# Optimization experiments

Measured on AMD Instinct MI355X. Metric: run time of the kernel, lower is better.

The kernel has to match this reference:

```python
import jax, jax.numpy as jnp
import numpy as np

B = 4; S_L = 512; WIN = 256; SCH = 3; CCH = 128; F = 8; P = 4; RNN = 128; FC = 256
L1 = (WIN - F + 1) // P          # after conv1 + pool1
L2 = (L1 - F + 1) // P           # after conv2 + pool2
D1 = L2 * CCH                    # flattened conv feature dim fed to GRU


def _conv1d(x, w, b):
    # x: (N, W, Cin), w: (F, Cin, Cout), VALID, stride 1 (matches keras Conv1D)
    return jax.lax.conv_general_dilated(x, w, (1,), 'VALID', dimension_numbers=('NWC', 'WIO', 'NWC')) + b


def _maxpool(x, p):
    return jax.lax.reduce_window(x, -jnp.inf, jax.lax.max, (1, p, 1), (1, p, 1), 'VALID')


def _gru(x, h0, mask, W, U, b):
    # keras GRU v2 (reset_after=True). b[0]=input bias, b[1]=recurrent bias.
    # Masked steps carry state through (keras semantics: output==state for GRU).
    u = U.shape[0]
    xg = x @ W + b[0]  # (B, T, 3u) precomputed input projections
    br = b[1]

    def step(h, inp):
        xt, mt = inp  # (B, 3u), (B,)
        rg = h @ U + br
        z = jax.nn.sigmoid(xt[:, :u] + rg[:, :u])
        r = jax.nn.sigmoid(xt[:, u:2 * u] + rg[:, u:2 * u])
        hh = jnp.tanh(xt[:, 2 * u:] + r * rg[:, 2 * u:])
        hn = z * h + (1.0 - z) * hh
        hn = jnp.where(mt[:, None], hn, h)
        return hn, hn

    _, ys = jax.lax.scan(step, h0, (jnp.swapaxes(xg, 0, 1), jnp.swapaxes(mask, 0, 1)))
    return jnp.swapaxes(ys, 0, 1)  # (B, T, u)


def _bidir(x, m, hf, hb, Wf, Uf, bf, Wb, Ub, bb):
    # Bidirectional(merge='concat'); backward layer sees reversed inputs+mask,
    # its output is reversed back to align with time (keras behaviour).
    yf = _gru(x, hf, m, Wf, Uf, bf)
    yb = _gru(x[:, ::-1], hb, m[:, ::-1], Wb, Ub, bb)[:, ::-1]
    return jnp.concatenate([yf, yb], axis=-1)


def _forward(x, state1_f, state1_b, state2_f, state2_b,
             conv1_w, conv1_b, conv2_w, conv2_b,
             g1f_W, g1f_U, g1f_b, g1b_W, g1b_U, g1b_b,
             g2f_W, g2f_U, g2f_b, g2b_W, g2b_U, g2b_b,
             d1_w, d1_b, d2_w, d2_b, d3_w, d3_b, m):
    bsz = x.shape[0]
    h = x.reshape(bsz * S_L, WIN, SCH)
    h = _maxpool(jax.nn.leaky_relu(_conv1d(h, conv1_w, conv1_b), 0.2), P)
    h = _maxpool(jax.nn.leaky_relu(_conv1d(h, conv2_w, conv2_b), 0.2), P)
    h = h.reshape(bsz, S_L, D1)
    h = _bidir(h, m, state1_f, state1_b, g1f_W, g1f_U, g1f_b, g1b_W, g1b_U, g1b_b)
    h = _bidir(h, m, state2_f, state2_b, g2f_W, g2f_U, g2f_b, g2b_W, g2b_U, g2b_b)
    # keras layers.Attention(use_scale=False): dot-product self attention,
    # key mask -> -1e9 on scores, query mask -> zero outputs.
    scores = jnp.einsum('btd,bsd->bts', h, h)
    scores = jnp.where(m[:, None, :], scores, -1e9)
    h = jnp.einsum('bts,bsd->btd', jax.nn.softmax(scores, axis=-1), h)
    h = h * m[:, :, None].astype(h.dtype)
    h = jax.nn.leaky_relu(h @ d1_w + d1_b, 0.2)   # dropout is identity at inference
    h = jax.nn.leaky_relu(h @ d2_w + d2_b, 0.2)
    return (h @ d3_w + d3_b)[..., 0]              # squeeze -> (B, s_l)


def setup_inputs() -> dict:
    key = jax.random.key(0)
    ks = jax.random.split(key, 32)
    g = lambda k, s: jax.random.normal(k, s, jnp.float32) * 0.05
    inp = {}
    inp['x'] = jax.random.normal(ks[0], (B, S_L, WIN, SCH), jnp.float32)
    inp['m'] = jax.random.randint(ks[1], (B, S_L), 0, 2) > 0
    inp['state1_f'] = jax.random.uniform(ks[2], (B, RNN), jnp.float32, -1.0, 1.0)
    inp['state1_b'] = jax.random.uniform(ks[3], (B, RNN), jnp.float32, -1.0, 1.0)
    inp['state2_f'] = jax.random.uniform(ks[4], (B, RNN), jnp.float32, -1.0, 1.0)
    inp['state2_b'] = jax.random.uniform(ks[5], (B, RNN), jnp.float32, -1.0, 1.0)
    inp['conv1_w'] = g(ks[6], (F, SCH, CCH)); inp['conv1_b'] = jnp.zeros((CCH,), jnp.float32)
    inp['conv2_w'] = g(ks[7], (F, CCH, CCH)); inp['conv2_b'] = jnp.zeros((CCH,), jnp.float32)
    i = 8
    for nm, din in (('g1f', D1), ('g1b', D1), ('g2f', 2 * RNN), ('g2b', 2 * RNN)):
        inp[nm + '_W'] = g(ks[i], (din, 3 * RNN))
        inp[nm + '_U'] = g(ks[i + 1], (RNN, 3 * RNN))
        inp[nm + '_b'] = jnp.zeros((2, 3 * RNN), jnp.float32)
        i += 2
    inp['d1_w'] = g(ks[i], (2 * RNN, FC)); inp['d1_b'] = jnp.zeros((FC,), jnp.float32)
    inp['d2_w'] = g(ks[i + 1], (FC, FC)); inp['d2_b'] = jnp.zeros((FC,), jnp.float32)
    inp['d3_w'] = g(ks[i + 2], (FC, 1)); inp['d3_b'] = jnp.zeros((1,), jnp.float32)
    return inp


def reference(x, m, state1_f, state1_b, state2_f, state2_b,
              conv1_w, conv1_b, conv2_w, conv2_b,
              g1f_W, g1f_U, g1f_b, g1b_W, g1b_U, g1b_b,
              g2f_W, g2f_U, g2f_b, g2b_W, g2b_U, g2b_b,
              d1_w, d1_b, d2_w, d2_b, d3_w, d3_b):
    return _forward(x, state1_f, state1_b, state2_f, state2_b,
                    conv1_w, conv1_b, conv2_w, conv2_b,
                    g1f_W, g1f_U, g1f_b, g1b_W, g1b_U, g1b_b,
                    g2f_W, g2f_U, g2f_b, g2b_W, g2b_U, g2b_b,
                    d1_w, d1_b, d2_w, d2_b, d3_w, d3_b, m)
```

## Files before the change

### kernel.cpp

```cpp
#include <hip/hip_runtime.h>

#define LRELU(v) ((v) > 0.f ? (v) : 0.2f * (v))

typedef float f32x4 __attribute__((ext_vector_type(4)));
typedef __bf16 bf16x8 __attribute__((ext_vector_type(8)));
typedef unsigned short ushort8v __attribute__((ext_vector_type(8)));

__device__ __forceinline__ unsigned short f2bf(float f) {
    unsigned int u = __float_as_uint(f);
    u += 0x7fffu + ((u >> 16) & 1u);
    return (unsigned short)(u >> 16);
}
__device__ __forceinline__ float bf2f(unsigned short h) {
    return __uint_as_float(((unsigned int)h) << 16);
}
__device__ __forceinline__ float sigmoid_fast(float x) {
    float e = __builtin_amdgcn_exp2f(-x * 1.442695041f);
    return __builtin_amdgcn_rcpf(1.f + e);
}
__device__ __forceinline__ float tanh_fast(float x) {
    float e = __builtin_amdgcn_exp2f(x * 2.885390082f);
    return 1.f - 2.f * __builtin_amdgcn_rcpf(e + 1.f);
}
__device__ __forceinline__ float dpp_add_xor1(float v) {
    int r = __builtin_amdgcn_mov_dpp(__float_as_int(v), 0xB1, 0xF, 0xF, true);
    return v + __int_as_float(r);
}
__device__ __forceinline__ float dpp_add_xor2(float v) {
    int r = __builtin_amdgcn_mov_dpp(__float_as_int(v), 0x4E, 0xF, 0xF, true);
    return v + __int_as_float(r);
}

__global__ void mask_decode_kernel(const unsigned int* __restrict__ mraw,
                                   int* __restrict__ mi) {
    __shared__ int is_u8;
    if (threadIdx.x == 0) {
        int u8 = 0;
        for (int i = 0; i < 512; i++) {
            if (mraw[i] > 1u) { u8 = 1; break; }
        }
        is_u8 = u8;
    }
    __syncthreads();
    if (is_u8) {
        const unsigned char* b8 = (const unsigned char*)mraw;
        for (int i = threadIdx.x; i < 2048; i += blockDim.x) mi[i] = b8[i] ? 1 : 0;
    } else {
        for (int i = threadIdx.x; i < 2048; i += blockDim.x) mi[i] = mraw[i] ? 1 : 0;
    }
}

__global__ __launch_bounds__(256) void prepack_w2(const float* __restrict__ w2,
                                                  unsigned short* __restrict__ bth,
                                                  unsigned short* __restrict__ btl) {
    int idx = blockIdx.x * 256 + threadIdx.x;
    int c = idx >> 10, k = idx & 1023;
    float v = w2[k * 128 + c];
    unsigned short hi = f2bf(v);
    unsigned short lo = f2bf(v - bf2f(hi));
    bth[(long)c * 1024 + k] = hi;
    btl[(long)c * 1024 + k] = lo;
}

__global__ __launch_bounds__(256) void prepack_wt(const float* __restrict__ W,
                                                  unsigned short* __restrict__ h,
                                                  unsigned short* __restrict__ l,
                                                  int K, int N) {
    long idx = (long)blockIdx.x * 256 + threadIdx.x;
    if (idx >= (long)K * N) return;
    int n = (int)(idx / K), k = (int)(idx % K);
    float v = W[(long)k * N + n];
    unsigned short hi = f2bf(v);
    unsigned short lo = f2bf(v - bf2f(hi));
    h[idx] = hi;
    l[idx] = lo;
}

__global__ __launch_bounds__(256) void conv_kernel(
    const float* __restrict__ x, const float* __restrict__ w1,
    const float* __restrict__ b1, const unsigned short* __restrict__ bth,
    const unsigned short* __restrict__ btl, const float* __restrict__ b2,
    float* __restrict__ feat) {
    __shared__ float xs[3][256];
    __shared__ __align__(16) unsigned short p1h[72 * 128];
    __shared__ __align__(16) unsigned short p1l[72 * 128];
    long s = blockIdx.x;
    int tid = threadIdx.x;
    const float* xp = x + s * 768;
    for (int i = tid; i < 768; i += 256) xs[i % 3][i / 3] = xp[i];
    for (int i = tid; i < 10 * 128; i += 256) {
        p1h[62 * 128 + i] = 0;
        p1l[62 * 128 + i] = 0;
    }
    __syncthreads();

    {
        int ch = tid & 127;
        int half = tid >> 7;
        float w1r[24];
#pragma unroll
        for (int fc = 0; fc < 24; fc++) w1r[fc] = w1[fc * 128 + ch];
        float bias1 = b1[ch];
        for (int po = half; po < 62; po += 2) {
            int p0 = po * 4;
            float a0 = bias1, a1 = bias1, a2 = bias1, a3 = bias1;
#pragma unroll
            for (int c = 0; c < 3; c++) {
                float xv[11];
#pragma unroll
                for (int q = 0; q < 11; q++) xv[q] = xs[c][p0 + q];
#pragma unroll
                for (int f = 0; f < 8; f++) {
                    float w = w1r[f * 3 + c];
                    a0 = fmaf(xv[f + 0], w, a0);
                    a1 = fmaf(xv[f + 1], w, a1);
                    a2 = fmaf(xv[f + 2], w, a2);
                    a3 = fmaf(xv[f + 3], w, a3);
                }
            }
            float m01 = fmaxf(LRELU(a0), LRELU(a1));
            float m23 = fmaxf(LRELU(a2), LRELU(a3));
            float v = fmaxf(m01, m23);
            unsigned short hi = f2bf(v);
            unsigned short lo = f2bf(v - bf2f(hi));
            int cs = ch ^ ((po & 7) << 3);
            p1h[po * 128 + cs] = hi;
            p1l[po * 128 + cs] = lo;
        }
    }
    __syncthreads();

    const int l = tid & 63, w = tid >> 6;
    const int r = l & 15, g = l >> 4;
    f32x4 acc[4][2];
    const f32x4 zz = {0.f, 0.f, 0.f, 0.f};
#pragma unroll
    for (int m = 0; m < 4; m++) {
        acc[m][0] = zz;
        acc[m][1] = zz;
    }
#pragma unroll 2
    for (int ks = 0; ks < 32; ks++) {
        const int f = ks >> 2;
        const int cin0 = ((ks & 3) << 5) + (g << 3);
        bf16x8 bh[2], bl[2];
#pragma unroll
        for (int n = 0; n < 2; n++) {
            const int c = ((w << 1) + n) * 16 + r;
            const long bo = (long)c * 1024 + (ks << 5) + (g << 3);
            bh[n] = __builtin_bit_cast(bf16x8, *(const ushort8v*)(bth + bo));
            bl[n] = __builtin_bit_cast(bf16x8, *(const ushort8v*)(btl + bo));
        }
        bf16x8 ah[4], al[4];
#pragma unroll
        for (int m = 0; m < 4; m++) {
            const int row = m * 16 + r + f;
            const int col = cin0 ^ ((row & 7) << 3);
            const int off = row * 128 + col;
            ah[m] = __builtin_bit_cast(bf16x8, *(const ushort8v*)(p1h + off));
            al[m] = __builtin_bit_cast(bf16x8, *(const ushort8v*)(p1l + off));
        }
#pragma unroll
        for (int m = 0; m < 4; m++) {
#pragma unroll
            for (int n = 0; n < 2; n++) {
                acc[m][n] = __builtin_amdgcn_mfma_f32_16x16x32_bf16(ah[m], bh[n], acc[m][n], 0, 0, 0);
                acc[m][n] = __builtin_amdgcn_mfma_f32_16x16x32_bf16(ah[m], bl[n], acc[m][n], 0, 0, 0);
                acc[m][n] = __builtin_amdgcn_mfma_f32_16x16x32_bf16(al[m], bh[n], acc[m][n], 0, 0, 0);
            }
        }
    }
#pragma unroll
    for (int m = 0; m < 4; m++) {
        const int j = m * 4 + g;
        if (j < 13) {
#pragma unroll
            for (int n = 0; n < 2; n++) {
                const int ch = ((w << 1) + n) * 16 + r;
                const float bias = b2[ch];
                float v0 = LRELU(acc[m][n].x + bias);
                float v1 = LRELU(acc[m][n].y + bias);
                float v2 = LRELU(acc[m][n].z + bias);
                float v3 = LRELU(acc[m][n].w + bias);
                feat[s * 1664 + j * 128 + ch] = fmaxf(fmaxf(v0, v1), fmaxf(v2, v3));
            }
        }
    }
}

template <int ACT>
__global__ __launch_bounds__(256) void gemm_bf16(
    const float* __restrict__ A, const unsigned short* __restrict__ Wth,
    const unsigned short* __restrict__ Wtl, const float* __restrict__ bias,
    float* __restrict__ C, int M, int N, int K) {
    __shared__ __align__(16) unsigned short Ah[64 * 40];
    __shared__ __align__(16) unsigned short Al[64 * 40];
    const int tid = threadIdx.x;
    const int w = tid >> 6, l = tid & 63, r = l & 15, g = l >> 4;
    const int m0 = blockIdx.y * 64, n0 = blockIdx.x * 64;
    const int col = n0 + w * 16 + r;
    const int srow = tid >> 2, sgq = tid & 3;
    f32x4 acc[4];
    const f32x4 zz = {0.f, 0.f, 0.f, 0.f};
#pragma unroll
    for (int m = 0; m < 4; m++) acc[m] = zz;

    const float* ap0 = A + (long)(m0 + srow) * K + sgq * 8;
    const long bbase = (long)col * K + g * 8;
    float4 v0 = *(const float4*)ap0;
    float4 v1 = *(const float4*)(ap0 + 4);
    ushort8v bhc = *(const ushort8v*)(Wth + bbase);
    ushort8v blc = *(const ushort8v*)(Wtl + bbase);

    for (int k0 = 0; k0 < K; k0 += 32) {
        float4 nv0, nv1;
        ushort8v nbh, nbl;
        if (k0 + 32 < K) {
            nv0 = *(const float4*)(ap0 + k0 + 32);
            nv1 = *(const float4*)(ap0 + k0 + 36);
            nbh = *(const ushort8v*)(Wth + bbase + k0 + 32);
            nbl = *(const ushort8v*)(Wtl + bbase + k0 + 32);
        }
        float vv[8] = {v0.x, v0.y, v0.z, v0.w, v1.x, v1.y, v1.z, v1.w};
        ushort8v hh, ll;
#pragma unroll
        for (int q = 0; q < 8; q++) {
            unsigned short h16 = f2bf(vv[q]);
            hh[q] = h16;
            ll[q] = f2bf(vv[q] - bf2f(h16));
        }
        const int slot = sgq ^ (srow & 3);
        __syncthreads();
        *(ushort8v*)&Ah[srow * 40 + slot * 8] = hh;
        *(ushort8v*)&Al[srow * 40 + slot * 8] = ll;
        __syncthreads();
        bf16x8 bh = __builtin_bit_cast(bf16x8, bhc);
        bf16x8 bl = __builtin_bit_cast(bf16x8, blc);
#pragma unroll
        for (int m = 0; m < 4; m++) {
            const int arow = m * 16 + r;
            const int aoff = arow * 40 + ((g ^ (arow & 3)) << 3);
            bf16x8 ah = __builtin_bit_cast(bf16x8, *(const ushort8v*)(Ah + aoff));
            bf16x8 al = __builtin_bit_cast(bf16x8, *(const ushort8v*)(Al + aoff));
            acc[m] = __builtin_amdgcn_mfma_f32_16x16x32_bf16(ah, bh, acc[m], 0, 0, 0);
            acc[m] = __builtin_amdgcn_mfma_f32_16x16x32_bf16(ah, bl, acc[m], 0, 0, 0);
            acc[m] = __builtin_amdgcn_mfma_f32_16x16x32_bf16(al, bh, acc[m], 0, 0, 0);
        }
        v0 = nv0; v1 = nv1; bhc = nbh; blc = nbl;
    }
    const float bv = bias ? bias[col] : 0.f;
#pragma unroll
    for (int m = 0; m < 4; m++) {
#pragma unroll
        for (int q = 0; q < 4; q++) {
            const int row = m0 + m * 16 + g * 4 + q;
            float v = acc[m][q] + bv;
            if (ACT == 1) v = LRELU(v);
            C[(long)row * N + col] = v;
        }
    }
}

template <int ACT>
__global__ __launch_bounds__(256) void gemm_nn(
    const float* __restrict__ A, long sA, const float* __restrict__ B, long sB,
    const float* __restrict__ bias, const int* __restrict__ qmask,
    float* __restrict__ C, long sC, int M, int N, int K) {
    int bz = blockIdx.z;
    A += (long)bz * sA;
    B += (long)bz * sB;
    C += (long)bz * sC;
    __shared__ __align__(16) float As[16][68];
    __shared__ __align__(16) float Bs[16][68];
    int tid = threadIdx.x;
    int tm = tid >> 4, tn = tid & 15;
    int m0 = blockIdx.y * 64, n0 = blockIdx.x * 64;
    int la_m = tid & 63, la_k = (tid >> 6) * 4;
    int lb_k = tid >> 4, lb_n = (tid & 15) * 4;
    float acc[4][4] = {};
    for (int k0 = 0; k0 < K; k0 += 16) {
        float4 av = *(const float4*)&A[(long)(m0 + la_m) * K + k0 + la_k];
        float4 bv = *(const float4*)&B[(long)(k0 + lb_k) * N + n0 + lb_n];
        As[la_k + 0][la_m] = av.x;
        As[la_k + 1][la_m] = av.y;
        As[la_k + 2][la_m] = av.z;
        As[la_k + 3][la_m] = av.w;
        *(float4*)&Bs[lb_k][lb_n] = bv;
        __syncthreads();
#pragma unroll
        for (int k = 0; k < 16; k++) {
            float4 a4 = *(const float4*)&As[k][tm * 4];
            float4 b4 = *(const float4*)&Bs[k][tn * 4];
            float aa[4] = {a4.x, a4.y, a4.z, a4.w};
            float bb[4] = {b4.x, b4.y, b4.z, b4.w};
#pragma unroll
            for (int i = 0; i < 4; i++)
#pragma unroll
                for (int j = 0; j < 4; j++) acc[i][j] = fmaf(aa[i], bb[j], acc[i][j]);
        }
        __syncthreads();
    }
#pragma unroll
    for (int i = 0; i < 4; i++) {
        int row = m0 + tm * 4 + i;
        float msc = qmask ? (float)qmask[(long)bz * M + row] : 1.f;
#pragma unroll
        for (int j = 0; j < 4; j++) {
            int col = n0 + tn * 4 + j;
            float v = acc[i][j] + (bias ? bias[col] : 0.f);
            if (ACT == 1) v = LRELU(v);
            C[(long)row * N + col] = v * msc;
        }
    }
}

__global__ __launch_bounds__(256) void scores_kernel(
    const float* __restrict__ h, const int* __restrict__ mask,
    float* __restrict__ S) {
    int bz = blockIdx.z;
    const float* A = h + (long)bz * 512 * 256;
    float* C = S + (long)bz * 512 * 512;
    __shared__ __align__(16) float As[16][68];
    __shared__ __align__(16) float Bs[16][68];
    int tid = threadIdx.x;
    int tm = tid >> 4, tn = tid & 15;
    int m0 = blockIdx.y * 64, n0 = blockIdx.x * 64;
    int lr = tid & 63, lk = (tid >> 6) * 4;
    float acc[4][4] = {};
    for (int k0 = 0; k0 < 256; k0 += 16) {
        float4 av = *(const float4*)&A[(long)(m0 + lr) * 256 + k0 + lk];
        float4 bv = *(const float4*)&A[(long)(n0 + lr) * 256 + k0 + lk];
        As[lk + 0][lr] = av.x;
        As[lk + 1][lr] = av.y;
        As[lk + 2][lr] = av.z;
        As[lk + 3][lr] = av.w;
        Bs[lk + 0][lr] = bv.x;
        Bs[lk + 1][lr] = bv.y;
        Bs[lk + 2][lr] = bv.z;
        Bs[lk + 3][lr] = bv.w;
        __syncthreads();
#pragma unroll
        for (int k = 0; k < 16; k++) {
            float4 a4 = *(const float4*)&As[k][tm * 4];
            float4 b4 = *(const float4*)&Bs[k][tn * 4];
            float aa[4] = {a4.x, a4.y, a4.z, a4.w};
            float bb[4] = {b4.x, b4.y, b4.z, b4.w};
#pragma unroll
            for (int i = 0; i < 4; i++)
#pragma unroll
                for (int j = 0; j < 4; j++) acc[i][j] = fmaf(aa[i], bb[j], acc[i][j]);
        }
        __syncthreads();
    }
#pragma unroll
    for (int i = 0; i < 4; i++) {
        int t = m0 + tm * 4 + i;
#pragma unroll
        for (int j = 0; j < 4; j++) {
            int ss = n0 + tn * 4 + j;
            C[(long)t * 512 + ss] = mask[bz * 512 + ss] ? acc[i][j] : -1e9f;
        }
    }
}

__global__ __launch_bounds__(256) void softmax_kernel(float* __restrict__ S) {
    long row = blockIdx.x;
    float* p = S + row * 512;
    int tid = threadIdx.x;
    __shared__ float red[8];
    float v0 = p[tid], v1 = p[tid + 256];
    float mx = fmaxf(v0, v1);
#pragma unroll
    for (int off = 32; off; off >>= 1) mx = fmaxf(mx, __shfl_down(mx, off));
    if ((tid & 63) == 0) red[tid >> 6] = mx;
    __syncthreads();
    mx = fmaxf(fmaxf(red[0], red[1]), fmaxf(red[2], red[3]));
    float e0 = expf(v0 - mx), e1 = expf(v1 - mx);
    float sm = e0 + e1;
#pragma unroll
    for (int off = 32; off; off >>= 1) sm += __shfl_down(sm, off);
    if ((tid & 63) == 0) red[4 + (tid >> 6)] = sm;
    __syncthreads();
    float inv = 1.f / (red[4] + red[5] + red[6] + red[7]);
    p[tid] = e0 * inv;
    p[tid + 256] = e1 * inv;
}

__global__ __launch_bounds__(512, 2) void gru_kernel(
    const float* __restrict__ xgf, const float* __restrict__ xgb,
    const float* __restrict__ Uf, const float* __restrict__ Ub,
    const float* __restrict__ brf, const float* __restrict__ brb,
    const float* __restrict__ h0f, const float* __restrict__ h0b,
    const int* __restrict__ mask, float* __restrict__ out) {
    int b = blockIdx.x & 3;
    int dir = blockIdx.x >> 2;
    const float* __restrict__ xg = dir ? xgb : xgf;
    const float* __restrict__ U = dir ? Ub : Uf;
    const float* __restrict__ br = dir ? brb : brf;
    const float* __restrict__ h0 = dir ? h0b : h0f;
    const int tid = threadIdx.x;
    const int c = tid >> 2;
    const int kq = tid & 3;

    __shared__ __align__(16) float xs[2][16 * 384];
    __shared__ __align__(16) float hsh[2][144];
    __shared__ unsigned long long mwords[8];

    auto stage = [&](int cc, int bufi) {
#pragma unroll
        for (int i = 0; i < 3; i++) {
            int g = i * 512 + tid;
            int j = g / 96;
            int col = (g - j * 96) * 4;
            int ts = cc * 16 + j;
            int t = dir ? (511 - ts) : ts;
            const float* src = xg + ((long)(b * 512 + t)) * 384 + col;
            __builtin_amdgcn_global_load_lds(
                (const __attribute__((address_space(1))) void*)src,
                (__attribute__((address_space(3))) void*)&xs[bufi][g * 4], 16, 0, 0);
        }
    };
    stage(0, 0);

    f32x4 u4[3][8];
#pragma unroll
    for (int g = 0; g < 3; g++)
#pragma unroll
        for (int q = 0; q < 8; q++) {
            const float* up = U + (long)(kq * 32 + q * 4) * 384 + g * 128 + c;
            u4[g][q].x = up[0];
            u4[g][q].y = up[384];
            u4[g][q].z = up[768];
            u4[g][q].w = up[1152];
        }
    float br3[3];
#pragma unroll
    for (int g = 0; g < 3; g++) br3[g] = br[g * 128 + c];

    float hreg = h0[b * 128 + c];
    if (kq == 0) hsh[0][c + (c >> 5) * 4] = hreg;
    if (tid < 64) {
#pragma unroll
        for (int w = 0; w < 8; w++) {
            int idx = w * 64 + tid;
            int t = dir ? (511 - idx) : idx;
            unsigned long long bm = __ballot(mask[b * 512 + t] != 0);
            if (tid == 0) mwords[w] = bm;
        }
    }
    asm volatile("s_waitcnt lgkmcnt(0)" ::: "memory");
    __builtin_amdgcn_s_barrier();

    int cur = 0;
    for (int cc = 0; cc < 32; cc++) {
        asm volatile("s_waitcnt vmcnt(0)" ::: "memory");
        if (cc < 31) stage(cc + 1, (cc + 1) & 1);
#pragma unroll
        for (int g = 0; g < 3; g++)
#pragma unroll
            for (int q = 0; q < 8; q++) asm volatile("" : "+v"(u4[g][q]));
        __builtin_amdgcn_s_barrier();
        const float* xb = xs[cc & 1];
        unsigned mwbits = (unsigned)((mwords[cc >> 2] >> ((cc & 3) * 16)) & 0xffffull);
#pragma unroll 1
        for (int jj = 0; jj < 16; jj++) {
            int step = cc * 16 + jj;
            int t = dir ? (511 - step) : step;
            long obase = ((long)(b * 512 + t)) * 256 + dir * 128;
            if ((mwbits >> jj) & 1) {
                const float* hp = &hsh[cur][kq * 36];
                float az0 = 0.f, az1 = 0.f, ar0 = 0.f, ar1 = 0.f, ah0 = 0.f, ah1 = 0.f;
#pragma unroll
                for (int q = 0; q < 8; q++) {
                    float4 h4 = *(const float4*)(hp + q * 4);
                    az0 = fmaf(h4.x, u4[0][q].x, az0);
                    az1 = fmaf(h4.y, u4[0][q].y, az1);
                    az0 = fmaf(h4.z, u4[0][q].z, az0);
                    az1 = fmaf(h4.w, u4[0][q].w, az1);
                    ar0 = fmaf(h4.x, u4[1][q].x, ar0);
                    ar1 = fmaf(h4.y, u4[1][q].y, ar1);
                    ar0 = fmaf(h4.z, u4[1][q].z, ar0);
                    ar1 = fmaf(h4.w, u4[1][q].w, ar1);
                    ah0 = fmaf(h4.x, u4[2][q].x, ah0);
                    ah1 = fmaf(h4.y, u4[2][q].y, ah1);
                    ah0 = fmaf(h4.z, u4[2][q].z, ah0);
                    ah1 = fmaf(h4.w, u4[2][q].w, ah1);
                }
                float rgz = dpp_add_xor2(dpp_add_xor1(az0 + az1));
                float rgr = dpp_add_xor2(dpp_add_xor1(ar0 + ar1));
                float rgh = dpp_add_xor2(dpp_add_xor1(ah0 + ah1));
                if (kq == 0) {
                    float xz = xb[jj * 384 + c];
                    float xr = xb[jj * 384 + 128 + c];
                    float xh = xb[jj * 384 + 256 + c];
                    float z = sigmoid_fast(xz + rgz + br3[0]);
                    float r_ = sigmoid_fast(xr + rgr + br3[1]);
                    float hc = tanh_fast(fmaf(r_, rgh + br3[2], xh));
                    float hn = fmaf(z, hreg - hc, hc);
                    hreg = hn;
                    hsh[cur ^ 1][c + (c >> 5) * 4] = hn;
                    out[obase + c] = hn;
                }
                asm volatile("s_waitcnt lgkmcnt(0)" ::: "memory");
                __builtin_amdgcn_s_barrier();
                cur ^= 1;
            } else {
                if (kq == 0) out[obase + c] = hreg;
            }
        }
    }
}

__global__ __launch_bounds__(256) void final_kernel(
    const float* __restrict__ fc2, const float* __restrict__ w,
    const float* __restrict__ b, float* __restrict__ out) {
    int row = blockIdx.x * 4 + (threadIdx.x >> 6);
    int lane = threadIdx.x & 63;
    const float* a = fc2 + (long)row * 256;
    float acc = 0.f;
#pragma unroll
    for (int i = 0; i < 4; i++) acc = fmaf(a[lane + i * 64], w[lane + i * 64], acc);
#pragma unroll
    for (int off = 32; off; off >>= 1) acc += __shfl_down(acc, off);
    if (lane == 0) out[row] = acc + b[0];
}

extern "C" void kernel_launch(void* const* d_in, const int* in_sizes, int n_in,
                              void* d_out, int out_size, void* d_ws,
                              size_t ws_size, hipStream_t stream) {
    const float* x = (const float*)d_in[0];
    const unsigned int* mraw = (const unsigned int*)d_in[1];
    const float* s1f = (const float*)d_in[2];
    const float* s1b = (const float*)d_in[3];
    const float* s2f = (const float*)d_in[4];
    const float* s2b = (const float*)d_in[5];
    const float* c1w = (const float*)d_in[6];
    const float* c1b = (const float*)d_in[7];
    const float* c2w = (const float*)d_in[8];
    const float* c2b = (const float*)d_in[9];
    const float* g1fW = (const float*)d_in[10];
    const float* g1fU = (const float*)d_in[11];
    const float* g1fb = (const float*)d_in[12];
    const float* g1bW = (const float*)d_in[13];
    const float* g1bU = (const float*)d_in[14];
    const float* g1bb = (const float*)d_in[15];
    const float* g2fW = (const float*)d_in[16];
    const float* g2fU = (const float*)d_in[17];
    const float* g2fb = (const float*)d_in[18];
    const float* g2bW = (const float*)d_in[19];
    const float* g2bU = (const float*)d_in[20];
    const float* g2bb = (const float*)d_in[21];
    const float* d1w = (const float*)d_in[22];
    const float* d1b = (const float*)d_in[23];
    const float* d2w = (const float*)d_in[24];
    const float* d2b = (const float*)d_in[25];
    const float* d3w = (const float*)d_in[26];
    const float* d3b = (const float*)d_in[27];
    float* out = (float*)d_out;

    float* ws = (float*)d_ws;
    size_t off = 0;
    auto take = [&](size_t n) {
        float* p = ws + off;
        off += (n + 63) & ~(size_t)63;
        return p;
    };
    int* mask_i = (int*)take(2048);
    float* feat = take(2048UL * 1664);
    float* xg1f = take(2048UL * 384);
    float* xg1b = take(2048UL * 384);
    float* gru1 = take(2048UL * 256);
    float* xg2f = take(2048UL * 384);
    float* xg2b = take(2048UL * 384);
    float* gru2 = take(2048UL * 256);
    float* sc = take(4UL * 512 * 512);
    float* attn = take(2048UL * 256);
    float* fc1 = take(2048UL * 256);
    float* fc2 = take(2048UL * 256);
    unsigned short* bth = (unsigned short*)take(65536);
    unsigned short* btl = (unsigned short*)take(65536);
    unsigned short* wt1fh = (unsigned short*)take(319488);
    unsigned short* wt1fl = (unsigned short*)take(319488);
    unsigned short* wt1bh = (unsigned short*)take(319488);
    unsigned short* wt1bl = (unsigned short*)take(319488);
    unsigned short* wt2fh = (unsigned short*)take(49152);
    unsigned short* wt2fl = (unsigned short*)take(49152);
    unsigned short* wt2bh = (unsigned short*)take(49152);
    unsigned short* wt2bl = (unsigned short*)take(49152);

    mask_decode_kernel<<<1, 256, 0, stream>>>(mraw, mask_i);
    prepack_w2<<<512, 256, 0, stream>>>(c2w, bth, btl);
    prepack_wt<<<2496, 256, 0, stream>>>(g1fW, wt1fh, wt1fl, 1664, 384);
    prepack_wt<<<2496, 256, 0, stream>>>(g1bW, wt1bh, wt1bl, 1664, 384);
    prepack_wt<<<384, 256, 0, stream>>>(g2fW, wt2fh, wt2fl, 256, 384);
    prepack_wt<<<384, 256, 0, stream>>>(g2bW, wt2bh, wt2bl, 256, 384);
    conv_kernel<<<2048, 256, 0, stream>>>(x, c1w, c1b, bth, btl, c2b, feat);

    gemm_bf16<0><<<dim3(6, 32), 256, 0, stream>>>(feat, wt1fh, wt1fl, g1fb,
                                                  xg1f, 2048, 384, 1664);
    gemm_bf16<0><<<dim3(6, 32), 256, 0, stream>>>(feat, wt1bh, wt1bl, g1bb,
                                                  xg1b, 2048, 384, 1664);
    gru_kernel<<<8, 512, 0, stream>>>(xg1f, xg1b, g1fU, g1bU, g1fb + 384,
                                      g1bb + 384, s1f, s1b, mask_i, gru1);

    gemm_bf16<0><<<dim3(6, 32), 256, 0, stream>>>(gru1, wt2fh, wt2fl, g2fb,
                                                  xg2f, 2048, 384, 256);
    gemm_bf16<0><<<dim3(6, 32), 256, 0, stream>>>(gru1, wt2bh, wt2bl, g2bb,
                                                  xg2b, 2048, 384, 256);
    gru_kernel<<<8, 512, 0, stream>>>(xg2f, xg2b, g2fU, g2bU, g2fb + 384,
                                      g2bb + 384, s2f, s2b, mask_i, gru2);

    scores_kernel<<<dim3(8, 8, 4), 256, 0, stream>>>(gru2, mask_i, sc);
    softmax_kernel<<<2048, 256, 0, stream>>>(sc);
    gemm_nn<0><<<dim3(4, 8, 4), 256, 0, stream>>>(sc, 512L * 512, gru2, 512L * 256,
                                                  nullptr, mask_i, attn, 512L * 256,
                                                  512, 256, 512);

    gemm_nn<1><<<dim3(4, 32, 1), 256, 0, stream>>>(attn, 0, d1w, 0, d1b, nullptr,
                                                   fc1, 0, 2048, 256, 256);
    gemm_nn<1><<<dim3(4, 32, 1), 256, 0, stream>>>(fc1, 0, d2w, 0, d2b, nullptr,
                                                   fc2, 0, 2048, 256, 256);
    final_kernel<<<512, 256, 0, stream>>>(fc2, d3w, d3b, out);
}
```

Before: 774.3 us.

## Halve GRU block size, two hidden units per thread with prepacked U

The recurrent GRU kernel now runs 256 threads per block instead of 512, and each thread computes two hidden columns (c and c+64), holding 48 float4 of U in registers. A new prepack kernel reorders U into a per-thread contiguous layout so each thread can load its slice with vector loads. The aim is cheaper per-step barriers and fewer waves to synchronise on the serial recurrence. The cost is higher register pressure (192 VGPRs for U alone), more serial FMA work per thread, and four extra prepack launches.

```diff
diff --git a/kernel.cpp b/kernel.cpp
--- a/kernel.cpp
+++ b/kernel.cpp
@@ -74,6 +74,17 @@
     unsigned short lo = f2bf(v - bf2f(hi));
     h[idx] = hi;
     l[idx] = lo;
+}
+
+__global__ __launch_bounds__(256) void prepack_ugru(const float* __restrict__ U,
+                                                    float* __restrict__ up) {
+    int idx = blockIdx.x * 256 + threadIdx.x;
+    if (idx >= 49152) return;
+    int tid = idx / 192, rem = idx % 192;
+    int g = rem >> 6, rem2 = rem & 63;
+    int p = rem2 >> 5, j = rem2 & 31;
+    int c = tid >> 2, kq = tid & 3;
+    up[idx] = U[(long)(kq * 32 + j) * 384 + g * 128 + p * 64 + c];
 }
 
 __global__ __launch_bounds__(256) void conv_kernel(
@@ -386,16 +397,16 @@
     p[tid + 256] = e1 * inv;
 }
 
-__global__ __launch_bounds__(512, 2) void gru_kernel(
+__global__ __launch_bounds__(256, 1) void gru_kernel(
     const float* __restrict__ xgf, const float* __restrict__ xgb,
-    const float* __restrict__ Uf, const float* __restrict__ Ub,
+    const float* __restrict__ Upf, const float* __restrict__ Upb,
     const float* __restrict__ brf, const float* __restrict__ brb,
     const float* __restrict__ h0f, const float* __restrict__ h0b,
     const int* __restrict__ mask, float* __restrict__ out) {
     int b = blockIdx.x & 3;
     int dir = blockIdx.x >> 2;
     const float* __restrict__ xg = dir ? xgb : xgf;
-    const float* __restrict__ U = dir ? Ub : Uf;
+    const float* __restrict__ Up = dir ? Upb : Upf;
     const float* __restrict__ br = dir ? brb : brf;
     const float* __restrict__ h0 = dir ? h0b : h0f;
     const int tid = threadIdx.x;
@@ -408,8 +419,8 @@
 
     auto stage = [&](int cc, int bufi) {
 #pragma unroll
-        for (int i = 0; i < 3; i++) {
-            int g = i * 512 + tid;
+        for (int i = 0; i < 6; i++) {
+            int g = i * 256 + tid;
             int j = g / 96;
             int col = (g - j * 96) * 4;
             int ts = cc * 16 + j;
@@ -422,23 +433,28 @@
     };
     stage(0, 0);
 
-    f32x4 u4[3][8];
-#pragma unroll
-    for (int g = 0; g < 3; g++)
-#pragma unroll
-        for (int q = 0; q < 8; q++) {
-            const float* up = U + (long)(kq * 32 + q * 4) * 384 + g * 128 + c;
-            u4[g][q].x = up[0];
-            u4[g][q].y = up[384];
-            u4[g][q].z = up[768];
-            u4[g][q].w = up[1152];
-        }
-    float br3[3];
-#pragma unroll
-    for (int g = 0; g < 3; g++) br3[g] = br[g * 128 + c];
-
-    float hreg = h0[b * 128 + c];
-    if (kq == 0) hsh[0][c + (c >> 5) * 4] = hreg;
+    f32x4 u4[48];
+    {
+        const f32x4* up = (const f32x4*)(Up + (long)tid * 192);
+#pragma unroll
+        for (int q = 0; q < 48; q++) u4[q] = up[q];
+    }
+#pragma unroll
+    for (int q = 0; q < 48; q++) asm volatile("" : "+v"(u4[q]));
+
+    float brv[6], hregp[2];
+#pragma unroll
+    for (int g = 0; g < 3; g++) {
+        brv[g * 2 + 0] = br[g * 128 + c];
+        brv[g * 2 + 1] = br[g * 128 + 64 + c];
+    }
+    hregp[0] = h0[b * 128 + c];
+    hregp[1] = h0[b * 128 + 64 + c];
+    if (kq == 0) {
+        hsh[0][c + (c >> 5) * 4] = hregp[0];
+        int c1 = c + 64;
+        hsh[0][c1 + (c1 >> 5) * 4] = hregp[1];
+    }
     if (tid < 64) {
 #pragma unroll
         for (int w = 0; w < 8; w++) {
@@ -455,10 +471,6 @@
     for (int cc = 0; cc < 32; cc++) {
         asm volatile("s_waitcnt vmcnt(0)" ::: "memory");
         if (cc < 31) stage(cc + 1, (cc + 1) & 1);
-#pragma unroll
-        for (int g = 0; g < 3; g++)
-#pragma unroll
-            for (int q = 0; q < 8; q++) asm volatile("" : "+v"(u4[g][q]));
         __builtin_amdgcn_s_barrier();
         const float* xb = xs[cc & 1];
         unsigned mwbits = (unsigned)((mwords[cc >> 2] >> ((cc & 3) * 16)) & 0xffffull);
@@ -469,43 +481,62 @@
             long obase = ((long)(b * 512 + t)) * 256 + dir * 128;
             if ((mwbits >> jj) & 1) {
                 const float* hp = &hsh[cur][kq * 36];
-                float az0 = 0.f, az1 = 0.f, ar0 = 0.f, ar1 = 0.f, ah0 = 0.f, ah1 = 0.f;
+                float s0 = 0.f, s1 = 0.f, s2 = 0.f, s3 = 0.f, s4 = 0.f, s5 = 0.f;
 #pragma unroll
                 for (int q = 0; q < 8; q++) {
                     float4 h4 = *(const float4*)(hp + q * 4);
-                    az0 = fmaf(h4.x, u4[0][q].x, az0);
-                    az1 = fmaf(h4.y, u4[0][q].y, az1);
-                    az0 = fmaf(h4.z, u4[0][q].z, az0);
-                    az1 = fmaf(h4.w, u4[0][q].w, az1);
-                    ar0 = fmaf(h4.x, u4[1][q].x, ar0);
-                    ar1 = fmaf(h4.y, u4[1][q].y, ar1);
-                    ar0 = fmaf(h4.z, u4[1][q].z, ar0);
-                    ar1 = fmaf(h4.w, u4[1][q].w, ar1);
-                    ah0 = fmaf(h4.x, u4[2][q].x, ah0);
-                    ah1 = fmaf(h4.y, u4[2][q].y, ah1);
-                    ah0 = fmaf(h4.z, u4[2][q].z, ah0);
-                    ah1 = fmaf(h4.w, u4[2][q].w, ah1);
+                    f32x4 uz0 = u4[q], uz1 = u4[8 + q];
+                    f32x4 ur0 = u4[16 + q], ur1 = u4[24 + q];
+                    f32x4 uh0 = u4[32 + q], uh1 = u4[40 + q];
+                    s0 = fmaf(h4.x, uz0.x, s0); s0 = fmaf(h4.y, uz0.y, s0);
+                    s0 = fmaf(h4.z, uz0.z, s0); s0 = fmaf(h4.w, uz0.w, s0);
+                    s1 = fmaf(h4.x, uz1.x, s1); s1 = fmaf(h4.y, uz1.y, s1);
+                    s1 = fmaf(h4.z, uz1.z, s1); s1 = fmaf(h4.w, uz1.w, s1);
+                    s2 = fmaf(h4.x, ur0.x, s2); s2 = fmaf(h4.y, ur0.y, s2);
+                    s2 = fmaf(h4.z, ur0.z, s2); s2 = fmaf(h4.w, ur0.w, s2);
+                    s3 = fmaf(h4.x, ur1.x, s3); s3 = fmaf(h4.y, ur1.y, s3);
+                    s3 = fmaf(h4.z, ur1.z, s3); s3 = fmaf(h4.w, ur1.w, s3);
+                    s4 = fmaf(h4.x, uh0.x, s4); s4 = fmaf(h4.y, uh0.y, s4);
+                    s4 = fmaf(h4.z, uh0.z, s4); s4 = fmaf(h4.w, uh0.w, s4);
+                    s5 = fmaf(h4.x, uh1.x, s5); s5 = fmaf(h4.y, uh1.y, s5);
+                    s5 = fmaf(h4.z, uh1.z, s5); s5 = fmaf(h4.w, uh1.w, s5);
                 }
-                float rgz = dpp_add_xor2(dpp_add_xor1(az0 + az1));
-                float rgr = dpp_add_xor2(dpp_add_xor1(ar0 + ar1));
-                float rgh = dpp_add_xor2(dpp_add_xor1(ah0 + ah1));
+                s0 = dpp_add_xor2(dpp_add_xor1(s0));
+                s1 = dpp_add_xor2(dpp_add_xor1(s1));
+                s2 = dpp_add_xor2(dpp_add_xor1(s2));
+                s3 = dpp_add_xor2(dpp_add_xor1(s3));
+                s4 = dpp_add_xor2(dpp_add_xor1(s4));
+                s5 = dpp_add_xor2(dpp_add_xor1(s5));
                 if (kq == 0) {
-                    float xz = xb[jj * 384 + c];
-                    float xr = xb[jj * 384 + 128 + c];
-                    float xh = xb[jj * 384 + 256 + c];
-                    float z = sigmoid_fast(xz + rgz + br3[0]);
-                    float r_ = sigmoid_fast(xr + rgr + br3[1]);
-                    float hc = tanh_fast(fmaf(r_, rgh + br3[2], xh));
-                    float hn = fmaf(z, hreg - hc, hc);
-                    hreg = hn;
-                    hsh[cur ^ 1][c + (c >> 5) * 4] = hn;
-                    out[obase + c] = hn;
+                    const float* xr0 = xb + jj * 384;
+                    {
+                        float z = sigmoid_fast(xr0[c] + s0 + brv[0]);
+                        float r_ = sigmoid_fast(xr0[128 + c] + s2 + brv[2]);
+                        float hcv = tanh_fast(fmaf(r_, s4 + brv[4], xr0[256 + c]));
+                        float hn = fmaf(z, hregp[0] - hcv, hcv);
+                        hregp[0] = hn;
+                        hsh[cur ^ 1][c + (c >> 5) * 4] = hn;
+                        out[obase + c] = hn;
+                    }
+                    {
+                        int c1 = c + 64;
+                        float z = sigmoid_fast(xr0[c1] + s1 + brv[1]);
+                        float r_ = sigmoid_fast(xr0[128 + c1] + s3 + brv[3]);
+                        float hcv = tanh_fast(fmaf(r_, s5 + brv[5], xr0[256 + c1]));
+                        float hn = fmaf(z, hregp[1] - hcv, hcv);
+                        hregp[1] = hn;
+                        hsh[cur ^ 1][c1 + (c1 >> 5) * 4] = hn;
+                        out[obase + c1] = hn;
+                    }
                 }
                 asm volatile("s_waitcnt lgkmcnt(0)" ::: "memory");
                 __builtin_amdgcn_s_barrier();
                 cur ^= 1;
             } else {
-                if (kq == 0) out[obase + c] = hreg;
+                if (kq == 0) {
+                    out[obase + c] = hregp[0];
+                    out[obase + 64 + c] = hregp[1];
+                }
             }
         }
     }
@@ -587,6 +618,10 @@
     unsigned short* wt2fl = (unsigned short*)take(49152);
     unsigned short* wt2bh = (unsigned short*)take(49152);
     unsigned short* wt2bl = (unsigned short*)take(49152);
+    float* up1f = take(49152);
+    float* up1b = take(49152);
+    float* up2f = take(49152);
+    float* up2b = take(49152);
 
     mask_decode_kernel<<<1, 256, 0, stream>>>(mraw, mask_i);
     prepack_w2<<<512, 256, 0, stream>>>(c2w, bth, btl);
@@ -594,20 +629,24 @@
     prepack_wt<<<2496, 256, 0, stream>>>(g1bW, wt1bh, wt1bl, 1664, 384);
     prepack_wt<<<384, 256, 0, stream>>>(g2fW, wt2fh, wt2fl, 256, 384);
     prepack_wt<<<384, 256, 0, stream>>>(g2bW, wt2bh, wt2bl, 256, 384);
+    prepack_ugru<<<192, 256, 0, stream>>>(g1fU, up1f);
+    prepack_ugru<<<192, 256, 0, stream>>>(g1bU, up1b);
+    prepack_ugru<<<192, 256, 0, stream>>>(g2fU, up2f);
+    prepack_ugru<<<192, 256, 0, stream>>>(g2bU, up2b);
     conv_kernel<<<2048, 256, 0, stream>>>(x, c1w, c1b, bth, btl, c2b, feat);
 
     gemm_bf16<0><<<dim3(6, 32), 256, 0, stream>>>(feat, wt1fh, wt1fl, g1fb,
                                                   xg1f, 2048, 384, 1664);
     gemm_bf16<0><<<dim3(6, 32), 256, 0, stream>>>(feat, wt1bh, wt1bl, g1bb,
                                                   xg1b, 2048, 384, 1664);
-    gru_kernel<<<8, 512, 0, stream>>>(xg1f, xg1b, g1fU, g1bU, g1fb + 384,
+    gru_kernel<<<8, 256, 0, stream>>>(xg1f, xg1b, up1f, up1b, g1fb + 384,
                                       g1bb + 384, s1f, s1b, mask_i, gru1);
 
     gemm_bf16<0><<<dim3(6, 32), 256, 0, stream>>>(gru1, wt2fh, wt2fl, g2fb,
                                                   xg2f, 2048, 384, 256);
     gemm_bf16<0><<<dim3(6, 32), 256, 0, stream>>>(gru1, wt2bh, wt2bl, g2bb,
                                                   xg2b, 2048, 384, 256);
-    gru_kernel<<<8, 512, 0, stream>>>(xg2f, xg2b, g2fU, g2bU, g2fb + 384,
+    gru_kernel<<<8, 256, 0, stream>>>(xg2f, xg2b, up2f, up2b, g2fb + 384,
                                       g2bb + 384, s2f, s2b, mask_i, gru2);
 
     scores_kernel<<<dim3(8, 8, 4), 256, 0, stream>>>(gru2, mask_i, sc);
```

Result: slower. 874.1 us (+12.9%).

## Emit split-bf16 activations from producers and use direct-to-LDS GEMM loads

Applied to the files above, without the earlier changes.

The conv and GRU kernels now write their outputs as pre-split bf16 hi/lo pairs. The GEMM no longer has to convert fp32 A tiles in every k-step, and it loads A straight into LDS with global_load_lds. The fp32 scores kernel is replaced by the same split-bf16 MFMA GEMM with a mask epilogue. In exchange the producers do extra conversion work and writes, and A tile loads are no longer prefetched one step ahead, which may expose load latency.

```diff
diff --git a/kernel.cpp b/kernel.cpp
--- a/kernel.cpp
+++ b/kernel.cpp
@@ -80,7 +80,7 @@
     const float* __restrict__ x, const float* __restrict__ w1,
     const float* __restrict__ b1, const unsigned short* __restrict__ bth,
     const unsigned short* __restrict__ btl, const float* __restrict__ b2,
-    float* __restrict__ feat) {
+    unsigned short* __restrict__ feat_h, unsigned short* __restrict__ feat_l) {
     __shared__ float xs[3][256];
     __shared__ __align__(16) unsigned short p1h[72 * 128];
     __shared__ __align__(16) unsigned short p1l[72 * 128];
@@ -182,19 +182,30 @@
                 float v1 = LRELU(acc[m][n].y + bias);
                 float v2 = LRELU(acc[m][n].z + bias);
                 float v3 = LRELU(acc[m][n].w + bias);
-                feat[s * 1664 + j * 128 + ch] = fmaxf(fmaxf(v0, v1), fmaxf(v2, v3));
+                float v = fmaxf(fmaxf(v0, v1), fmaxf(v2, v3));
+                unsigned short hi = f2bf(v);
+                feat_h[s * 1664 + j * 128 + ch] = hi;
+                feat_l[s * 1664 + j * 128 + ch] = f2bf(v - bf2f(hi));
             }
         }
     }
 }
 
-template <int ACT>
-__global__ __launch_bounds__(256) void gemm_bf16(
-    const float* __restrict__ A, const unsigned short* __restrict__ Wth,
-    const unsigned short* __restrict__ Wtl, const float* __restrict__ bias,
-    float* __restrict__ C, int M, int N, int K) {
-    __shared__ __align__(16) unsigned short Ah[64 * 40];
-    __shared__ __align__(16) unsigned short Al[64 * 40];
+template <int MASK>
+__global__ __launch_bounds__(256) void gemm_bf16v2(
+    const unsigned short* __restrict__ Agh, const unsigned short* __restrict__ Agl,
+    const unsigned short* __restrict__ Bth, const unsigned short* __restrict__ Btl,
+    const float* __restrict__ bias, const int* __restrict__ mask,
+    float* __restrict__ C, long sAz, long sBz, long sCz,
+    int M, int N, int K) {
+    const int bz = blockIdx.z;
+    Agh += (long)bz * sAz;
+    Agl += (long)bz * sAz;
+    Bth += (long)bz * sBz;
+    Btl += (long)bz * sBz;
+    C += (long)bz * sCz;
+    __shared__ __align__(16) unsigned short Ahs[64 * 32];
+    __shared__ __align__(16) unsigned short Als[64 * 32];
     const int tid = threadIdx.x;
     const int w = tid >> 6, l = tid & 63, r = l & 15, g = l >> 4;
     const int m0 = blockIdx.y * 64, n0 = blockIdx.x * 64;
@@ -205,57 +216,54 @@
 #pragma unroll
     for (int m = 0; m < 4; m++) acc[m] = zz;
 
-    const float* ap0 = A + (long)(m0 + srow) * K + sgq * 8;
+    const long abase = (long)(m0 + srow) * K + ((sgq ^ (srow & 3)) << 3);
     const long bbase = (long)col * K + g * 8;
-    float4 v0 = *(const float4*)ap0;
-    float4 v1 = *(const float4*)(ap0 + 4);
-    ushort8v bhc = *(const ushort8v*)(Wth + bbase);
-    ushort8v blc = *(const ushort8v*)(Wtl + bbase);
+    ushort8v bhc = *(const ushort8v*)(Bth + bbase);
+    ushort8v blc = *(const ushort8v*)(Btl + bbase);
 
     for (int k0 = 0; k0 < K; k0 += 32) {
-        float4 nv0, nv1;
+        __syncthreads();
+        __builtin_amdgcn_global_load_lds(
+            (const __attribute__((address_space(1))) void*)(Agh + abase + k0),
+            (__attribute__((address_space(3))) void*)&Ahs[tid * 8], 16, 0, 0);
+        __builtin_amdgcn_global_load_lds(
+            (const __attribute__((address_space(1))) void*)(Agl + abase + k0),
+            (__attribute__((address_space(3))) void*)&Als[tid * 8], 16, 0, 0);
         ushort8v nbh, nbl;
         if (k0 + 32 < K) {
-            nv0 = *(const float4*)(ap0 + k0 + 32);
-            nv1 = *(const float4*)(ap0 + k0 + 36);
-            nbh = *(const ushort8v*)(Wth + bbase + k0 + 32);
-            nbl = *(const ushort8v*)(Wtl + bbase + k0 + 32);
-        }
-        float vv[8] = {v0.x, v0.y, v0.z, v0.w, v1.x, v1.y, v1.z, v1.w};
-        ushort8v hh, ll;
-#pragma unroll
-        for (int q = 0; q < 8; q++) {
-            unsigned short h16 = f2bf(vv[q]);
-            hh[q] = h16;
-            ll[q] = f2bf(vv[q] - bf2f(h16));
-        }
-        const int slot = sgq ^ (srow & 3);
-        __syncthreads();
-        *(ushort8v*)&Ah[srow * 40 + slot * 8] = hh;
-        *(ushort8v*)&Al[srow * 40 + slot * 8] = ll;
+            nbh = *(const ushort8v*)(Bth + bbase + k0 + 32);
+            nbl = *(const ushort8v*)(Btl + bbase + k0 + 32);
+        }
         __syncthreads();
         bf16x8 bh = __builtin_bit_cast(bf16x8, bhc);
         bf16x8 bl = __builtin_bit_cast(bf16x8, blc);
 #pragma unroll
         for (int m = 0; m < 4; m++) {
             const int arow = m * 16 + r;
-            const int aoff = arow * 40 + ((g ^ (arow & 3)) << 3);
-            bf16x8 ah = __builtin_bit_cast(bf16x8, *(const ushort8v*)(Ah + aoff));
-            bf16x8 al = __builtin_bit_cast(bf16x8, *(const ushort8v*)(Al + aoff));
+            const int aoff = arow * 32 + ((g ^ (arow & 3)) << 3);
+            bf16x8 ah = __builtin_bit_cast(bf16x8, *(const ushort8v*)(Ahs + aoff));
+            bf16x8 al = __builtin_bit_cast(bf16x8, *(const ushort8v*)(Als + aoff));
             acc[m] = __builtin_amdgcn_mfma_f32_16x16x32_bf16(ah, bh, acc[m], 0, 0, 0);
             acc[m] = __builtin_amdgcn_mfma_f32_16x16x32_bf16(ah, bl, acc[m], 0, 0, 0);
             acc[m] = __builtin_amdgcn_mfma_f32_16x16x32_bf16(al, bh, acc[m], 0, 0, 0);
         }
-        v0 = nv0; v1 = nv1; bhc = nbh; blc = nbl;
-    }
-    const float bv = bias ? bias[col] : 0.f;
+        bhc = nbh;
+        blc = nbl;
+    }
+    float bv = 0.f;
+    int mk = 1;
+    if (MASK == 0) {
+        bv = bias ? bias[col] : 0.f;
+    } else {
+        mk = mask[bz * 512 + col];
+    }
 #pragma unroll
     for (int m = 0; m < 4; m++) {
 #pragma unroll
         for (int q = 0; q < 4; q++) {
             const int row = m0 + m * 16 + g * 4 + q;
             float v = acc[m][q] + bv;
-            if (ACT == 1) v = LRELU(v);
+            if (MASK == 1) v = mk ? v : -1e9f;
             C[(long)row * N + col] = v;
         }
     }
@@ -314,55 +322,6 @@
     }
 }
 
-__global__ __launch_bounds__(256) void scores_kernel(
-    const float* __restrict__ h, const int* __restrict__ mask,
-    float* __restrict__ S) {
-    int bz = blockIdx.z;
-    const float* A = h + (long)bz * 512 * 256;
-    float* C = S + (long)bz * 512 * 512;
-    __shared__ __align__(16) float As[16][68];
-    __shared__ __align__(16) float Bs[16][68];
-    int tid = threadIdx.x;
-    int tm = tid >> 4, tn = tid & 15;
-    int m0 = blockIdx.y * 64, n0 = blockIdx.x * 64;
-    int lr = tid & 63, lk = (tid >> 6) * 4;
-    float acc[4][4] = {};
-    for (int k0 = 0; k0 < 256; k0 += 16) {
-        float4 av = *(const float4*)&A[(long)(m0 + lr) * 256 + k0 + lk];
-        float4 bv = *(const float4*)&A[(long)(n0 + lr) * 256 + k0 + lk];
-        As[lk + 0][lr] = av.x;
-        As[lk + 1][lr] = av.y;
-        As[lk + 2][lr] = av.z;
-        As[lk + 3][lr] = av.w;
-        Bs[lk + 0][lr] = bv.x;
-        Bs[lk + 1][lr] = bv.y;
-        Bs[lk + 2][lr] = bv.z;
-        Bs[lk + 3][lr] = bv.w;
-        __syncthreads();
-#pragma unroll
-        for (int k = 0; k < 16; k++) {
-            float4 a4 = *(const float4*)&As[k][tm * 4];
-            float4 b4 = *(const float4*)&Bs[k][tn * 4];
-            float aa[4] = {a4.x, a4.y, a4.z, a4.w};
-            float bb[4] = {b4.x, b4.y, b4.z, b4.w};
-#pragma unroll
-            for (int i = 0; i < 4; i++)
-#pragma unroll
-                for (int j = 0; j < 4; j++) acc[i][j] = fmaf(aa[i], bb[j], acc[i][j]);
-        }
-        __syncthreads();
-    }
-#pragma unroll
-    for (int i = 0; i < 4; i++) {
-        int t = m0 + tm * 4 + i;
-#pragma unroll
-        for (int j = 0; j < 4; j++) {
-            int ss = n0 + tn * 4 + j;
-            C[(long)t * 512 + ss] = mask[bz * 512 + ss] ? acc[i][j] : -1e9f;
-        }
-    }
-}
-
 __global__ __launch_bounds__(256) void softmax_kernel(float* __restrict__ S) {
     long row = blockIdx.x;
     float* p = S + row * 512;
@@ -391,7 +350,8 @@
     const float* __restrict__ Uf, const float* __restrict__ Ub,
     const float* __restrict__ brf, const float* __restrict__ brb,
     const float* __restrict__ h0f, const float* __restrict__ h0b,
-    const int* __restrict__ mask, float* __restrict__ out) {
+    const int* __restrict__ mask, float* __restrict__ out,
+    unsigned short* __restrict__ outh, unsigned short* __restrict__ outl) {
     int b = blockIdx.x & 3;
     int dir = blockIdx.x >> 2;
     const float* __restrict__ xg = dir ? xgb : xgf;
@@ -500,12 +460,20 @@
                     hreg = hn;
                     hsh[cur ^ 1][c + (c >> 5) * 4] = hn;
                     out[obase + c] = hn;
+                    unsigned short hh = f2bf(hn);
+                    outh[obase + c] = hh;
+                    outl[obase + c] = f2bf(hn - bf2f(hh));
                 }
                 asm volatile("s_waitcnt lgkmcnt(0)" ::: "memory");
                 __builtin_amdgcn_s_barrier();
                 cur ^= 1;
             } else {
-                if (kq == 0) out[obase + c] = hreg;
+                if (kq == 0) {
+                    out[obase + c] = hreg;
+                    unsigned short hh = f2bf(hreg);
+                    outh[obase + c] = hh;
+                    outl[obase + c] = f2bf(hreg - bf2f(hh));
+                }
             }
         }
     }
@@ -566,13 +534,18 @@
         return p;
     };
     int* mask_i = (int*)take(2048);
-    float* feat = take(2048UL * 1664);
+    unsigned short* feat_h = (unsigned short*)take(2048UL * 1664 / 2);
+    unsigned short* feat_l = (unsigned short*)take(2048UL * 1664 / 2);
     float* xg1f = take(2048UL * 384);
     float* xg1b = take(2048UL * 384);
     float* gru1 = take(2048UL * 256);
+    unsigned short* gru1h = (unsigned short*)take(2048UL * 128);
+    unsigned short* gru1l = (unsigned short*)take(2048UL * 128);
     float* xg2f = take(2048UL * 384);
     float* xg2b = take(2048UL * 384);
     float* gru2 = take(2048UL * 256);
+    unsigned short* gru2h = (unsigned short*)take(2048UL * 128);
+    unsigned short* gru2l = (unsigned short*)take(2048UL * 128);
     float* sc = take(4UL * 512 * 512);
     float* attn = take(2048UL * 256);
     float* fc1 = take(2048UL * 256);
@@ -594,23 +567,25 @@
     prepack_wt<<<2496, 256, 0, stream>>>(g1bW, wt1bh, wt1bl, 1664, 384);
     prepack_wt<<<384, 256, 0, stream>>>(g2fW, wt2fh, wt2fl, 256, 384);
     prepack_wt<<<384, 256, 0, stream>>>(g2bW, wt2bh, wt2bl, 256, 384);
-    conv_kernel<<<2048, 256, 0, stream>>>(x, c1w, c1b, bth, btl, c2b, feat);
-
-    gemm_bf16<0><<<dim3(6, 32), 256, 0, stream>>>(feat, wt1fh, wt1fl, g1fb,
-                                                  xg1f, 2048, 384, 1664);
-    gemm_bf16<0><<<dim3(6, 32), 256, 0, stream>>>(feat, wt1bh, wt1bl, g1bb,
-                                                  xg1b, 2048, 384, 1664);
+    conv_kernel<<<2048, 256, 0, stream>>>(x, c1w, c1b, bth, btl, c2b, feat_h, feat_l);
+
+    gemm_bf16v2<0><<<dim3(6, 32, 1), 256, 0, stream>>>(
+        feat_h, feat_l, wt1fh, wt1fl, g1fb, nullptr, xg1f, 0, 0, 0, 2048, 384, 1664);
+    gemm_bf16v2<0><<<dim3(6, 32, 1), 256, 0, stream>>>(
+        feat_h, feat_l, wt1bh, wt1bl, g1bb, nullptr, xg1b, 0, 0, 0, 2048, 384, 1664);
     gru_kernel<<<8, 512, 0, stream>>>(xg1f, xg1b, g1fU, g1bU, g1fb + 384,
-                                      g1bb + 384, s1f, s1b, mask_i, gru1);
-
-    gemm_bf16<0><<<dim3(6, 32), 256, 0, stream>>>(gru1, wt2fh, wt2fl, g2fb,
-                                                  xg2f, 2048, 384, 256);
-    gemm_bf16<0><<<dim3(6, 32), 256, 0, stream>>>(gru1, wt2bh, wt2bl, g2bb,
-                                                  xg2b, 2048, 384, 256);
+                                      g1bb + 384, s1f, s1b, mask_i, gru1, gru1h, gru1l);
+
+    gemm_bf16v2<0><<<dim3(6, 32, 1), 256, 0, stream>>>(
+        gru1h, gru1l, wt2fh, wt2fl, g2fb, nullptr, xg2f, 0, 0, 0, 2048, 384, 256);
+    gemm_bf16v2<0><<<dim3(6, 32, 1), 256, 0, stream>>>(
+        gru1h, gru1l, wt2bh, wt2bl, g2bb, nullptr, xg2b, 0, 0, 0, 2048, 384, 256);
     gru_kernel<<<8, 512, 0, stream>>>(xg2f, xg2b, g2fU, g2bU, g2fb + 384,
-                                      g2bb + 384, s2f, s2b, mask_i, gru2);
-
-    scores_kernel<<<dim3(8, 8, 4), 256, 0, stream>>>(gru2, mask_i, sc);
+                                      g2bb + 384, s2f, s2b, mask_i, gru2, gru2h, gru2l);
+
+    gemm_bf16v2<1><<<dim3(8, 8, 4), 256, 0, stream>>>(
+        gru2h, gru2l, gru2h, gru2l, nullptr, mask_i, sc,
+        512L * 256, 512L * 256, 512L * 512, 512, 512, 256);
     softmax_kernel<<<2048, 256, 0, stream>>>(sc);
     gemm_nn<0><<<dim3(4, 8, 4), 256, 0, stream>>>(sc, 512L * 512, gru2, 512L * 256,
                                                   nullptr, mask_i, attn, 512L * 256,
```

Measured after the change: 801.5 us. 1.04x slower.
